# Optimization experiments

Measured on AMD Instinct MI355X. Metric: run time of the kernel, lower is better.

The kernel has to match this reference:

```python
import jax, jax.numpy as jnp
import numpy as np

N_NODES = 50000
N_EDGES = 800000
D_IN = 512
HIDDEN = 32
HEADS = 4
N_CLASSES = 40
NEG_SLOPE = 0.2


def gat_layer(x, W, a_src, a_dst, b, src, dst, num_nodes, concat):
    # x: [N, D], W: [D, H, C], a_src/a_dst: [H, C], b: [H*C] or [C]
    h = jnp.einsum('nd,dhc->nhc', x, W)  # [N, H, C]
    # attention logits per edge (edge j->i with j=src, i=dst)
    e = jnp.sum(h[src] * a_src, axis=-1) + jnp.sum(h[dst] * a_dst, axis=-1)  # [E, H]
    e = jnp.where(e > 0, e, NEG_SLOPE * e)  # leaky_relu
    # segment softmax over incoming edges of each dst node
    m = jax.ops.segment_max(e, dst, num_segments=num_nodes)  # [N, H]
    ex = jnp.exp(e - m[dst])
    denom = jax.ops.segment_sum(ex, dst, num_segments=num_nodes)
    alpha = ex / (denom[dst] + 1e-9)  # [E, H]
    # weighted scatter-aggregate of neighbor features
    out = jax.ops.segment_sum(alpha[:, :, None] * h[src], dst, num_segments=num_nodes)  # [N, H, C]
    if concat:
        out = out.reshape(num_nodes, -1)  # [N, H*C]
    else:
        out = out.mean(axis=1)  # [N, C]
    return out + b, alpha


def setup_inputs() -> dict:
    key = jax.random.key(0)
    ks = jax.random.split(key, 12)
    x = jax.random.normal(ks[0], (N_NODES, D_IN), dtype=jnp.float32)
    src = jax.random.randint(ks[1], (N_EDGES,), 0, N_NODES, dtype=jnp.int32)
    dst = jax.random.randint(ks[2], (N_EDGES,), 0, N_NODES, dtype=jnp.int32)
    s1 = 1.0 / np.sqrt(D_IN)
    W1 = jax.random.normal(ks[3], (D_IN, HEADS, HIDDEN), dtype=jnp.float32) * s1
    a_src1 = jax.random.normal(ks[4], (HEADS, HIDDEN), dtype=jnp.float32) * 0.1
    a_dst1 = jax.random.normal(ks[5], (HEADS, HIDDEN), dtype=jnp.float32) * 0.1
    b1 = jnp.zeros((HEADS * HIDDEN,), dtype=jnp.float32)
    d2 = HEADS * HIDDEN
    s2 = 1.0 / np.sqrt(d2)
    W2 = jax.random.normal(ks[6], (d2, 1, N_CLASSES), dtype=jnp.float32) * s2
    a_src2 = jax.random.normal(ks[7], (1, N_CLASSES), dtype=jnp.float32) * 0.1
    a_dst2 = jax.random.normal(ks[8], (1, N_CLASSES), dtype=jnp.float32) * 0.1
    b2 = jnp.zeros((N_CLASSES,), dtype=jnp.float32)
    return {"x": x, "src": src, "dst": dst,
            "W1": W1, "a_src1": a_src1, "a_dst1": a_dst1, "b1": b1,
            "W2": W2, "a_src2": a_src2, "a_dst2": a_dst2, "b2": b2}


def reference(x, src, dst, W1, a_src1, a_dst1, b1, W2, a_src2, a_dst2, b2):
    n = x.shape[0]
    # add self loops (standard in GATConv)
    loops = jnp.arange(n, dtype=src.dtype)
    s = jnp.concatenate([src, loops])
    d = jnp.concatenate([dst, loops])
    h1, _attn = gat_layer(x, W1, a_src1, a_dst1, b1, s, d, n, concat=True)
    h1 = jax.nn.elu(h1)
    h2, _ = gat_layer(h1, W2, a_src2, a_dst2, b2, s, d, n, concat=False)
    return jax.nn.softmax(h2, axis=-1)
```

## Files before the change

kernel.cpp:

```cpp
#include <hip/hip_runtime.h>
#include <hip/hip_bf16.h>
#include <math.h>

#define NN 50000
#define NE 800000
#define ET 850000
#define DIN 512
#define F1 128
#define NC 40
#define NEG 0.2f
#define CAP 128
#define SCAN_NB ((NN + 255) / 256)

typedef __attribute__((ext_vector_type(8))) short s16x8;
typedef __attribute__((ext_vector_type(4))) float f32x4;

__device__ inline unsigned short bfh(float f) {
    __hip_bfloat16 h = __float2bfloat16(f);
    return __builtin_bit_cast(unsigned short, h);
}
__device__ inline float bff(unsigned short u) {
    unsigned int x = (unsigned int)u << 16;
    return __builtin_bit_cast(float, x);
}

__device__ inline void split8(f32x4 v0, f32x4 v1, s16x8* hi, s16x8* lo) {
    float f[8] = {v0.x, v0.y, v0.z, v0.w, v1.x, v1.y, v1.z, v1.w};
    #pragma unroll
    for (int j = 0; j < 8; ++j) {
        unsigned short h = bfh(f[j]);
        (*hi)[j] = (short)h;
        (*lo)[j] = (short)bfh(f[j] - bff(h));
    }
}

__device__ inline void gl16(const void* g, void* l) {
    __builtin_amdgcn_global_load_lds((const __attribute__((address_space(1))) unsigned int*)g,
                                     (__attribute__((address_space(3))) unsigned int*)l, 16, 0, 0);
}

__global__ void prep_kernel(const float* __restrict__ W1,
        const float* __restrict__ W2, int* __restrict__ deg,
        unsigned short* __restrict__ Wh1T, unsigned short* __restrict__ Wl1T,
        unsigned short* __restrict__ Wh2T, unsigned short* __restrict__ Wl2T) {
    int i = blockIdx.x * blockDim.x + threadIdx.x;
    if (i < NN) deg[i] = 0;
    if (i < DIN * F1) {
        int k = i >> 7, c = i & 127;
        float w = W1[i];
        unsigned short h = bfh(w);
        unsigned short l = bfh(w - bff(h));
        Wh1T[c * DIN + k] = h;
        Wl1T[c * DIN + k] = l;
    }
    if (i < 48 * 128) {
        int c = i >> 7, k = i & 127;
        float w = (c < NC) ? W2[k * NC + c] : 0.f;
        unsigned short h = bfh(w);
        unsigned short l = bfh(w - bff(h));
        Wh2T[c * 128 + k] = h;
        Wl2T[c * 128 + k] = l;
    }
}

__global__ void hist_kernel(const int* __restrict__ dst, int* __restrict__ deg) {
    int e = blockIdx.x * blockDim.x + threadIdx.x;
    if (e >= ET) return;
    int d = (e < NE) ? dst[e] : (e - NE);
    atomicAdd(&deg[d], 1);
}

__global__ __launch_bounds__(256) void partial_kernel(const int* __restrict__ deg,
        int* __restrict__ bsum) {
    __shared__ int red[4];
    int i = blockIdx.x * 256 + threadIdx.x;
    int v = (i < NN) ? deg[i] : 0;
    #pragma unroll
    for (int o = 1; o < 64; o <<= 1) v += __shfl_xor(v, o);
    if ((threadIdx.x & 63) == 0) red[threadIdx.x >> 6] = v;
    __syncthreads();
    if (threadIdx.x == 0) bsum[blockIdx.x] = red[0] + red[1] + red[2] + red[3];
}

__global__ __launch_bounds__(256) void scanp_kernel(const int* __restrict__ bsum,
        int* __restrict__ bbase) {
    __shared__ int s[256];
    int t = threadIdx.x;
    s[t] = (t < SCAN_NB) ? bsum[t] : 0;
    __syncthreads();
    #pragma unroll
    for (int o = 1; o < 256; o <<= 1) {
        int v = (t >= o) ? s[t - o] : 0;
        __syncthreads();
        s[t] += v;
        __syncthreads();
    }
    if (t < SCAN_NB) bbase[t] = (t == 0) ? 0 : s[t - 1];
}

__global__ __launch_bounds__(256) void emit_kernel(const int* __restrict__ deg,
        const int* __restrict__ bbase, int* __restrict__ off, int* __restrict__ cur) {
    __shared__ int s[256];
    int t = threadIdx.x;
    int i = blockIdx.x * 256 + t;
    int d = (i < NN) ? deg[i] : 0;
    s[t] = d;
    __syncthreads();
    #pragma unroll
    for (int o = 1; o < 256; o <<= 1) {
        int v = (t >= o) ? s[t - o] : 0;
        __syncthreads();
        s[t] += v;
        __syncthreads();
    }
    int o0 = bbase[blockIdx.x] + s[t] - d;
    if (i < NN) { off[i] = o0; cur[i] = o0; }
    if (i == NN - 1) off[NN] = o0 + d;
}

__global__ void scatter_kernel(const int* __restrict__ src, const int* __restrict__ dst,
        int* __restrict__ cur, int* __restrict__ ssorted) {
    int e = blockIdx.x * blockDim.x + threadIdx.x;
    if (e >= ET) return;
    int s = (e < NE) ? src[e] : (e - NE);
    int d = (e < NE) ? dst[e] : (e - NE);
    int pos = atomicAdd(&cur[d], 1);
    ssorted[pos] = s;
}

__global__ __launch_bounds__(256) void gemm1_mfma(const float* __restrict__ X,
        const unsigned short* __restrict__ BhT, const unsigned short* __restrict__ BlT,
        const float* __restrict__ a_src, const float* __restrict__ a_dst,
        float* __restrict__ H, float* __restrict__ s1s, float* __restrict__ s1d) {
    __shared__ char lds[49152];
    char* ldsAh = lds;
    char* ldsAl = lds + 8192;
    char* ldsBh = lds + 16384;
    char* ldsBl = lds + 32768;
    const int tid = threadIdx.x;
    const int wid = tid >> 6, lane = tid & 63;
    const int wm = wid >> 1, wn = wid & 1;
    const int l15 = lane & 15, lg = lane >> 4;
    const int row0 = blockIdx.x * 64;

    const int arow = tid >> 2;
    const int akc  = (tid & 3) * 16;
    const int asw  = (arow & 7) << 4;
    int agr = row0 + arow; if (agr > NN - 1) agr = NN - 1;
    const float* aptr = X + (long)agr * DIN + akc;

    f32x4 acc[2][4];
    #pragma unroll
    for (int mi = 0; mi < 2; ++mi)
        #pragma unroll
        for (int ni = 0; ni < 4; ++ni) acc[mi][ni] = (f32x4)(0.f);

    for (int k0 = 0; k0 < DIN; k0 += 64) {
        #pragma unroll
        for (int p = 0; p < 4; ++p) {
            int q = p * 256 + tid;
            int dstoff = (p * 256 + wid * 64) << 4;
            int rr = q >> 3;
            int w = (q & 7) << 4;
            int sw = (rr & 7) << 4;
            long sb = (long)rr * (DIN * 2) + k0 * 2 + (w ^ sw);
            gl16((const char*)BhT + sb, ldsBh + dstoff);
            gl16((const char*)BlT + sb, ldsBl + dstoff);
        }
        {
            f32x4 v0 = *(const f32x4*)(aptr + k0);
            f32x4 v1 = *(const f32x4*)(aptr + k0 + 4);
            f32x4 v2 = *(const f32x4*)(aptr + k0 + 8);
            f32x4 v3 = *(const f32x4*)(aptr + k0 + 12);
            s16x8 h0, l0, h1, l1;
            split8(v0, v1, &h0, &l0);
            split8(v2, v3, &h1, &l1);
            int b0 = arow * 128 + ((akc * 2) ^ asw);
            int b1 = arow * 128 + ((akc * 2 + 16) ^ asw);
            *(s16x8*)(ldsAh + b0) = h0;
            *(s16x8*)(ldsAh + b1) = h1;
            *(s16x8*)(ldsAl + b0) = l0;
            *(s16x8*)(ldsAl + b1) = l1;
        }
        __syncthreads();
        #pragma unroll
        for (int ks = 0; ks < 2; ++ks) {
            s16x8 ah[2], al[2], bh[4], bl[4];
            #pragma unroll
            for (int mi = 0; mi < 2; ++mi) {
                int row = wm * 32 + mi * 16 + l15;
                int sw = (row & 7) << 4;
                int kb = (ks * 32 + lg * 8) * 2;
                ah[mi] = *(const s16x8*)(ldsAh + row * 128 + (kb ^ sw));
                al[mi] = *(const s16x8*)(ldsAl + row * 128 + (kb ^ sw));
            }
            #pragma unroll
            for (int ni = 0; ni < 4; ++ni) {
                int col = wn * 64 + ni * 16 + l15;
                int sw = (col & 7) << 4;
                int kb = (ks * 32 + lg * 8) * 2;
                bh[ni] = *(const s16x8*)(ldsBh + col * 128 + (kb ^ sw));
                bl[ni] = *(const s16x8*)(ldsBl + col * 128 + (kb ^ sw));
            }
            #pragma unroll
            for (int mi = 0; mi < 2; ++mi)
                #pragma unroll
                for (int ni = 0; ni < 4; ++ni) {
                    acc[mi][ni] = __builtin_amdgcn_mfma_f32_16x16x32_bf16(ah[mi], bh[ni], acc[mi][ni], 0, 0, 0);
                    acc[mi][ni] = __builtin_amdgcn_mfma_f32_16x16x32_bf16(ah[mi], bl[ni], acc[mi][ni], 0, 0, 0);
                    acc[mi][ni] = __builtin_amdgcn_mfma_f32_16x16x32_bf16(al[mi], bh[ni], acc[mi][ni], 0, 0, 0);
                }
        }
        __syncthreads();
    }

    #pragma unroll
    for (int mi = 0; mi < 2; ++mi)
        #pragma unroll
        for (int ni = 0; ni < 4; ++ni) {
            int col = wn * 64 + ni * 16 + l15;
            #pragma unroll
            for (int r = 0; r < 4; ++r) {
                int grow = row0 + wm * 32 + mi * 16 + lg * 4 + r;
                if (grow < NN) H[(long)grow * F1 + col] = acc[mi][ni][r];
            }
        }
    float av[4], bv[4];
    #pragma unroll
    for (int ni = 0; ni < 4; ++ni) {
        int col = wn * 64 + ni * 16 + l15;
        av[ni] = a_src[col];
        bv[ni] = a_dst[col];
    }
    #pragma unroll
    for (int mi = 0; mi < 2; ++mi)
        #pragma unroll
        for (int hl = 0; hl < 2; ++hl) {
            #pragma unroll
            for (int r = 0; r < 4; ++r) {
                float t1 = acc[mi][2 * hl][r] * av[2 * hl] + acc[mi][2 * hl + 1][r] * av[2 * hl + 1];
                float t2 = acc[mi][2 * hl][r] * bv[2 * hl] + acc[mi][2 * hl + 1][r] * bv[2 * hl + 1];
                #pragma unroll
                for (int o = 1; o < 16; o <<= 1) {
                    t1 += __shfl_xor(t1, o);
                    t2 += __shfl_xor(t2, o);
                }
                int grow = row0 + wm * 32 + mi * 16 + lg * 4 + r;
                if (l15 == 0 && grow < NN) {
                    int head = 2 * wn + hl;
                    s1s[grow * 4 + head] = t1;
                    s1d[grow * 4 + head] = t2;
                }
            }
        }
}

__global__ __launch_bounds__(256) void gemm2_mfma(const float* __restrict__ H1,
        const unsigned short* __restrict__ B2h, const unsigned short* __restrict__ B2l,
        const float* __restrict__ a_src, const float* __restrict__ a_dst,
        float* __restrict__ Z, float* __restrict__ s2s, float* __restrict__ s2d) {
    __shared__ char lds[57344];
    char* ldsA  = lds;
    char* ldsBh = lds + 32768;
    char* ldsBl = lds + 45056;
    const int tid = threadIdx.x;
    const int wid = tid >> 6, lane = tid & 63;
    const int l15 = lane & 15, lg = lane >> 4;
    const int row0 = blockIdx.x * 64;

    #pragma unroll
    for (int p = 0; p < 8; ++p) {
        int q = p * 256 + tid;
        int row = q >> 5;
        int w = (q & 31) << 4;
        int sw = (row & 7) << 4;
        int gr = row0 + row; if (gr > NN - 1) gr = NN - 1;
        gl16((const char*)(H1 + (long)gr * F1) + (w ^ sw), ldsA + ((p * 256 + wid * 64) << 4));
    }
    #pragma unroll
    for (int p = 0; p < 3; ++p) {
        int q = p * 256 + tid;
        int rr = q >> 4;
        int w = (q & 15) << 4;
        int sw = (rr & 7) << 4;
        int dstoff = (p * 256 + wid * 64) << 4;
        gl16((const char*)B2h + rr * 256 + (w ^ sw), ldsBh + dstoff);
        gl16((const char*)B2l + rr * 256 + (w ^ sw), ldsBl + dstoff);
    }
    __syncthreads();

    f32x4 acc[3];
    #pragma unroll
    for (int ni = 0; ni < 3; ++ni) acc[ni] = (f32x4)(0.f);

    #pragma unroll
    for (int ks = 0; ks < 4; ++ks) {
        int row = wid * 16 + l15;
        int sw = (row & 7) << 4;
        int kb = (ks * 32 + lg * 8) * 4;
        f32x4 v0 = *(const f32x4*)(ldsA + row * 512 + ((kb)      ^ sw));
        f32x4 v1 = *(const f32x4*)(ldsA + row * 512 + ((kb + 16) ^ sw));
        s16x8 ah, al;
        split8(v0, v1, &ah, &al);
        #pragma unroll
        for (int ni = 0; ni < 3; ++ni) {
            int cc = ni * 16 + l15;
            int swb = (cc & 7) << 4;
            int kb2 = (ks * 32 + lg * 8) * 2;
            s16x8 bh = *(const s16x8*)(ldsBh + cc * 256 + (kb2 ^ swb));
            s16x8 bl = *(const s16x8*)(ldsBl + cc * 256 + (kb2 ^ swb));
            acc[ni] = __builtin_amdgcn_mfma_f32_16x16x32_bf16(ah, bh, acc[ni], 0, 0, 0);
            acc[ni] = __builtin_amdgcn_mfma_f32_16x16x32_bf16(ah, bl, acc[ni], 0, 0, 0);
            acc[ni] = __builtin_amdgcn_mfma_f32_16x16x32_bf16(al, bh, acc[ni], 0, 0, 0);
        }
    }

    float av[3], bv[3];
    #pragma unroll
    for (int ni = 0; ni < 3; ++ni) {
        int cc = ni * 16 + l15;
        av[ni] = (cc < NC) ? a_src[cc] : 0.f;
        bv[ni] = (cc < NC) ? a_dst[cc] : 0.f;
    }
    #pragma unroll
    for (int r = 0; r < 4; ++r) {
        int grow = row0 + wid * 16 + lg * 4 + r;
        bool ok = grow < NN;
        float t1 = acc[0][r] * av[0] + acc[1][r] * av[1] + acc[2][r] * av[2];
        float t2 = acc[0][r] * bv[0] + acc[1][r] * bv[1] + acc[2][r] * bv[2];
        #pragma unroll
        for (int o = 1; o < 16; o <<= 1) {
            t1 += __shfl_xor(t1, o);
            t2 += __shfl_xor(t2, o);
        }
        #pragma unroll
        for (int ni = 0; ni < 3; ++ni) {
            int cc = ni * 16 + l15;
            if (ok && cc < NC) Z[(long)grow * NC + cc] = acc[ni][r];
        }
        if (ok && l15 == 0) { s2s[grow] = t1; s2d[grow] = t2; }
    }
}

__global__ __launch_bounds__(256) void fusedagg1_kernel(
        const int* __restrict__ off, const int* __restrict__ ssorted,
        const float* __restrict__ ssrc, const float* __restrict__ sdst,
        const float* __restrict__ H, const float* __restrict__ b,
        float* __restrict__ O) {
    __shared__ int idx_lds[4][CAP];
    __shared__ __align__(16) float e_lds[4][CAP][4];
    const int nd = threadIdx.x >> 6;
    int n = blockIdx.x * 4 + nd;
    if (n >= NN) return;
    const int lane = threadIdx.x & 63;
    const int base = off[n];
    const int deg  = off[n + 1] - base;
    const float4 vd = *(const float4*)(sdst + (long)n * 4);

    float m0 = -1e30f, m1 = -1e30f, m2 = -1e30f, m3 = -1e30f;
    for (int k = lane; k < deg; k += 64) {
        int s = ssorted[base + k];
        float4 vs = *(const float4*)(ssrc + (long)s * 4);
        float x0 = vs.x + vd.x; x0 = (x0 > 0.f) ? x0 : NEG * x0;
        float x1 = vs.y + vd.y; x1 = (x1 > 0.f) ? x1 : NEG * x1;
        float x2 = vs.z + vd.z; x2 = (x2 > 0.f) ? x2 : NEG * x2;
        float x3 = vs.w + vd.w; x3 = (x3 > 0.f) ? x3 : NEG * x3;
        if (k < CAP) {
            idx_lds[nd][k] = s;
            *(f32x4*)&e_lds[nd][k][0] = (f32x4){x0, x1, x2, x3};
        }
        m0 = fmaxf(m0, x0); m1 = fmaxf(m1, x1);
        m2 = fmaxf(m2, x2); m3 = fmaxf(m3, x3);
    }
    #pragma unroll
    for (int o = 1; o < 64; o <<= 1) {
        m0 = fmaxf(m0, __shfl_xor(m0, o));
        m1 = fmaxf(m1, __shfl_xor(m1, o));
        m2 = fmaxf(m2, __shfl_xor(m2, o));
        m3 = fmaxf(m3, __shfl_xor(m3, o));
    }
    float t0 = 0.f, t1 = 0.f, t2 = 0.f, t3 = 0.f;
    for (int k = lane; k < deg; k += 64) {
        float x0, x1, x2, x3;
        if (k < CAP) {
            f32x4 v = *(const f32x4*)&e_lds[nd][k][0];
            x0 = v.x; x1 = v.y; x2 = v.z; x3 = v.w;
        } else {
            int s = ssorted[base + k];
            float4 vs = *(const float4*)(ssrc + (long)s * 4);
            x0 = vs.x + vd.x; x0 = (x0 > 0.f) ? x0 : NEG * x0;
            x1 = vs.y + vd.y; x1 = (x1 > 0.f) ? x1 : NEG * x1;
            x2 = vs.z + vd.z; x2 = (x2 > 0.f) ? x2 : NEG * x2;
            x3 = vs.w + vd.w; x3 = (x3 > 0.f) ? x3 : NEG * x3;
        }
        float e0 = __expf(x0 - m0), e1 = __expf(x1 - m1);
        float e2 = __expf(x2 - m2), e3 = __expf(x3 - m3);
        if (k < CAP) *(f32x4*)&e_lds[nd][k][0] = (f32x4){e0, e1, e2, e3};
        t0 += e0; t1 += e1; t2 += e2; t3 += e3;
    }
    #pragma unroll
    for (int o = 1; o < 64; o <<= 1) {
        t0 += __shfl_xor(t0, o); t1 += __shfl_xor(t1, o);
        t2 += __shfl_xor(t2, o); t3 += __shfl_xor(t3, o);
    }
    const int g = lane >> 4;
    const int l = lane & 15;
    const int hd = l >> 2;
    const float mh  = (hd == 0) ? m0 : (hd == 1) ? m1 : (hd == 2) ? m2 : m3;
    const float th  = (hd == 0) ? t0 : (hd == 1) ? t1 : (hd == 2) ? t2 : t3;
    const float ih  = 1.f / (th + 1e-9f);
    const float vdh = (hd == 0) ? vd.x : (hd == 1) ? vd.y : (hd == 2) ? vd.z : vd.w;
    const int c0 = l * 8;
    f32x4 accA = (f32x4)(0.f), accB = (f32x4)(0.f);
    const int kend = (deg < CAP) ? deg : CAP;
    for (int k = g; k < kend; k += 4) {
        int s = idx_lds[nd][k];
        float e = e_lds[nd][k][hd];
        const float* hp = H + (long)s * F1 + c0;
        f32x4 h0 = *(const f32x4*)(hp);
        f32x4 h1 = *(const f32x4*)(hp + 4);
        accA += (f32x4)(e) * h0;
        accB += (f32x4)(e) * h1;
    }
    for (int k = CAP + g; k < deg; k += 4) {
        int s = ssorted[base + k];
        float4 vs = *(const float4*)(ssrc + (long)s * 4);
        float x = ((hd == 0) ? vs.x : (hd == 1) ? vs.y : (hd == 2) ? vs.z : vs.w) + vdh;
        x = (x > 0.f) ? x : NEG * x;
        float e = __expf(x - mh);
        const float* hp = H + (long)s * F1 + c0;
        f32x4 h0 = *(const f32x4*)(hp);
        f32x4 h1 = *(const f32x4*)(hp + 4);
        accA += (f32x4)(e) * h0;
        accB += (f32x4)(e) * h1;
    }
    #pragma unroll
    for (int o = 16; o < 64; o <<= 1) {
        accA.x += __shfl_xor(accA.x, o); accA.y += __shfl_xor(accA.y, o);
        accA.z += __shfl_xor(accA.z, o); accA.w += __shfl_xor(accA.w, o);
        accB.x += __shfl_xor(accB.x, o); accB.y += __shfl_xor(accB.y, o);
        accB.z += __shfl_xor(accB.z, o); accB.w += __shfl_xor(accB.w, o);
    }
    if (g == 0) {
        f32x4 bbA = *(const f32x4*)(b + c0);
        f32x4 bbB = *(const f32x4*)(b + c0 + 4);
        f32x4 vA = accA * (f32x4)(ih) + bbA;
        f32x4 vB = accB * (f32x4)(ih) + bbB;
        vA.x = (vA.x > 0.f) ? vA.x : expm1f(vA.x);
        vA.y = (vA.y > 0.f) ? vA.y : expm1f(vA.y);
        vA.z = (vA.z > 0.f) ? vA.z : expm1f(vA.z);
        vA.w = (vA.w > 0.f) ? vA.w : expm1f(vA.w);
        vB.x = (vB.x > 0.f) ? vB.x : expm1f(vB.x);
        vB.y = (vB.y > 0.f) ? vB.y : expm1f(vB.y);
        vB.z = (vB.z > 0.f) ? vB.z : expm1f(vB.z);
        vB.w = (vB.w > 0.f) ? vB.w : expm1f(vB.w);
        *(f32x4*)(O + (long)n * F1 + c0)     = vA;
        *(f32x4*)(O + (long)n * F1 + c0 + 4) = vB;
    }
}

__global__ __launch_bounds__(256) void fusedagg2_kernel(
        const int* __restrict__ off, const int* __restrict__ ssorted,
        const float* __restrict__ ssrc, const float* __restrict__ sdst,
        const float* __restrict__ Z, const float* __restrict__ b,
        float* __restrict__ out) {
    __shared__ int   idx_lds[4][CAP];
    __shared__ float e_lds[4][CAP];
    const int nd = threadIdx.x >> 6;
    int n = blockIdx.x * 4 + nd;
    if (n >= NN) return;
    const int lane = threadIdx.x & 63;
    const int base = off[n];
    const int deg  = off[n + 1] - base;
    const float sdn = sdst[n];

    float m = -1e30f;
    for (int k = lane; k < deg; k += 64) {
        int s = ssorted[base + k];
        float x = ssrc[s] + sdn;
        x = (x > 0.f) ? x : NEG * x;
        if (k < CAP) { idx_lds[nd][k] = s; e_lds[nd][k] = x; }
        m = fmaxf(m, x);
    }
    #pragma unroll
    for (int o = 1; o < 64; o <<= 1) m = fmaxf(m, __shfl_xor(m, o));
    float t = 0.f;
    for (int k = lane; k < deg; k += 64) {
        float x;
        if (k < CAP) x = e_lds[nd][k];
        else {
            int s = ssorted[base + k];
            x = ssrc[s] + sdn;
            x = (x > 0.f) ? x : NEG * x;
        }
        float e = __expf(x - m);
        if (k < CAP) e_lds[nd][k] = e;
        t += e;
    }
    #pragma unroll
    for (int o = 1; o < 64; o <<= 1) t += __shfl_xor(t, o);
    const float inv = 1.f / (t + 1e-9f);

    const int g = lane >> 3;
    const int l = lane & 7;
    const int c0 = l * 5;
    float a0 = 0.f, a1 = 0.f, a2 = 0.f, a3 = 0.f, a4 = 0.f;
    const int kend = (deg < CAP) ? deg : CAP;
    for (int k = g; k < kend; k += 8) {
        int s = idx_lds[nd][k];
        float e = e_lds[nd][k];
        const float* zp = Z + (long)s * NC + c0;
        a0 += e * zp[0]; a1 += e * zp[1]; a2 += e * zp[2];
        a3 += e * zp[3]; a4 += e * zp[4];
    }
    for (int k = CAP + g; k < deg; k += 8) {
        int s = ssorted[base + k];
        float x = ssrc[s] + sdn;
        x = (x > 0.f) ? x : NEG * x;
        float e = __expf(x - m);
        const float* zp = Z + (long)s * NC + c0;
        a0 += e * zp[0]; a1 += e * zp[1]; a2 += e * zp[2];
        a3 += e * zp[3]; a4 += e * zp[4];
    }
    #pragma unroll
    for (int o = 8; o < 64; o <<= 1) {
        a0 += __shfl_xor(a0, o); a1 += __shfl_xor(a1, o);
        a2 += __shfl_xor(a2, o); a3 += __shfl_xor(a3, o);
        a4 += __shfl_xor(a4, o);
    }
    if (g == 0) {
        float v0 = a0 * inv + b[c0 + 0];
        float v1 = a1 * inv + b[c0 + 1];
        float v2 = a2 * inv + b[c0 + 2];
        float v3 = a3 * inv + b[c0 + 3];
        float v4 = a4 * inv + b[c0 + 4];
        float mx = fmaxf(fmaxf(fmaxf(v0, v1), fmaxf(v2, v3)), v4);
        #pragma unroll
        for (int o = 1; o < 8; o <<= 1) mx = fmaxf(mx, __shfl_xor(mx, o));
        float e0 = __expf(v0 - mx), e1 = __expf(v1 - mx), e2 = __expf(v2 - mx);
        float e3 = __expf(v3 - mx), e4 = __expf(v4 - mx);
        float s = e0 + e1 + e2 + e3 + e4;
        #pragma unroll
        for (int o = 1; o < 8; o <<= 1) s += __shfl_xor(s, o);
        float is = 1.f / s;
        float* op = out + (long)n * NC + c0;
        op[0] = e0 * is; op[1] = e1 * is; op[2] = e2 * is;
        op[3] = e3 * is; op[4] = e4 * is;
    }
}

extern "C" void kernel_launch(void* const* d_in, const int* in_sizes, int n_in,
                              void* d_out, int out_size, void* d_ws, size_t ws_size,
                              hipStream_t stream) {
    const float* x      = (const float*)d_in[0];
    const int*   src    = (const int*)  d_in[1];
    const int*   dst    = (const int*)  d_in[2];
    const float* W1     = (const float*)d_in[3];
    const float* a_src1 = (const float*)d_in[4];
    const float* a_dst1 = (const float*)d_in[5];
    const float* b1     = (const float*)d_in[6];
    const float* W2     = (const float*)d_in[7];
    const float* a_src2 = (const float*)d_in[8];
    const float* a_dst2 = (const float*)d_in[9];
    const float* b2     = (const float*)d_in[10];
    float* out = (float*)d_out;

    float* ws   = (float*)d_ws;
    float* hpre = ws;
    float* s1s  = hpre + 6400000;
    float* s1d  = s1s + 200000;
    float* h1   = s1d + 200000;
    float* z2   = h1 + 6400000;
    float* s2s  = z2 + 2000000;
    float* s2d  = s2s + 50000;
    int*   deg     = (int*)(s2d + 50000);
    int*   off     = deg + 50000;
    int*   cur     = off + 50008;
    int*   ssorted = cur + 50000;
    int*   bsum    = ssorted + 850000;
    int*   bbase   = bsum + 256;
    unsigned short* Wh1T = (unsigned short*)(bbase + 256);
    unsigned short* Wl1T = Wh1T + 65536;
    unsigned short* Wh2T = Wl1T + 65536;
    unsigned short* Wl2T = Wh2T + 6144;

    prep_kernel<<<(DIN * F1 + 255) / 256, 256, 0, stream>>>(W1, W2, deg, Wh1T, Wl1T, Wh2T, Wl2T);

    hist_kernel<<<(ET + 255) / 256, 256, 0, stream>>>(dst, deg);
    partial_kernel<<<SCAN_NB, 256, 0, stream>>>(deg, bsum);
    scanp_kernel<<<1, 256, 0, stream>>>(bsum, bbase);
    emit_kernel<<<SCAN_NB, 256, 0, stream>>>(deg, bbase, off, cur);
    scatter_kernel<<<(ET + 255) / 256, 256, 0, stream>>>(src, dst, cur, ssorted);

    gemm1_mfma<<<(NN + 63) / 64, 256, 0, stream>>>(x, Wh1T, Wl1T, a_src1, a_dst1, hpre, s1s, s1d);
    fusedagg1_kernel<<<(NN + 3) / 4, 256, 0, stream>>>(off, ssorted, s1s, s1d, hpre, b1, h1);

    gemm2_mfma<<<(NN + 63) / 64, 256, 0, stream>>>(h1, Wh2T, Wl2T, a_src2, a_dst2, z2, s2s, s2d);
    fusedagg2_kernel<<<(NN + 3) / 4, 256, 0, stream>>>(off, ssorted, s2s, s2d, z2, b2, out);
}
```

Baseline: 401.2 us.

## Store node features as fp16 and pre-split aggregated hidden into bf16 hi/lo

The projected features H and Z are now stored in fp16 instead of fp32, which halves the bytes read by the random gathers in both aggregation kernels. The first aggregation kernel now writes its output as bf16 hi/lo pairs, so gemm2 loads ready-made operands and no longer splits fp32 values in LDS. This lowers gather bandwidth and gemm2 load work, at the cost of fp16 rounding in the intermediate features and a small precision risk in the final output.

```diff
diff --git a/kernel.cpp b/kernel.cpp
--- a/kernel.cpp
+++ b/kernel.cpp
@@ -14,6 +14,7 @@
 
 typedef __attribute__((ext_vector_type(8))) short s16x8;
 typedef __attribute__((ext_vector_type(4))) float f32x4;
+typedef __attribute__((ext_vector_type(8))) _Float16 f16x8;
 
 __device__ inline unsigned short bfh(float f) {
     __hip_bfloat16 h = __float2bfloat16(f);
@@ -131,7 +132,7 @@
 __global__ __launch_bounds__(256) void gemm1_mfma(const float* __restrict__ X,
         const unsigned short* __restrict__ BhT, const unsigned short* __restrict__ BlT,
         const float* __restrict__ a_src, const float* __restrict__ a_dst,
-        float* __restrict__ H, float* __restrict__ s1s, float* __restrict__ s1d) {
+        _Float16* __restrict__ H, float* __restrict__ s1s, float* __restrict__ s1d) {
     __shared__ char lds[49152];
     char* ldsAh = lds;
     char* ldsAl = lds + 8192;
@@ -222,7 +223,7 @@
             #pragma unroll
             for (int r = 0; r < 4; ++r) {
                 int grow = row0 + wm * 32 + mi * 16 + lg * 4 + r;
-                if (grow < NN) H[(long)grow * F1 + col] = acc[mi][ni][r];
+                if (grow < NN) H[(long)grow * F1 + col] = (_Float16)acc[mi][ni][r];
             }
         }
     float av[4], bv[4];
@@ -255,12 +256,14 @@
         }
 }
 
-__global__ __launch_bounds__(256) void gemm2_mfma(const float* __restrict__ H1,
+__global__ __launch_bounds__(256) void gemm2_mfma(
+        const unsigned short* __restrict__ H1h, const unsigned short* __restrict__ H1l,
         const unsigned short* __restrict__ B2h, const unsigned short* __restrict__ B2l,
         const float* __restrict__ a_src, const float* __restrict__ a_dst,
-        float* __restrict__ Z, float* __restrict__ s2s, float* __restrict__ s2d) {
+        _Float16* __restrict__ Z, float* __restrict__ s2s, float* __restrict__ s2d) {
     __shared__ char lds[57344];
-    char* ldsA  = lds;
+    char* ldsAh = lds;
+    char* ldsAl = lds + 16384;
     char* ldsBh = lds + 32768;
     char* ldsBl = lds + 45056;
     const int tid = threadIdx.x;
@@ -269,13 +272,15 @@
     const int row0 = blockIdx.x * 64;
 
     #pragma unroll
-    for (int p = 0; p < 8; ++p) {
+    for (int p = 0; p < 4; ++p) {
         int q = p * 256 + tid;
-        int row = q >> 5;
-        int w = (q & 31) << 4;
-        int sw = (row & 7) << 4;
-        int gr = row0 + row; if (gr > NN - 1) gr = NN - 1;
-        gl16((const char*)(H1 + (long)gr * F1) + (w ^ sw), ldsA + ((p * 256 + wid * 64) << 4));
+        int rr = q >> 4;
+        int w = (q & 15) << 4;
+        int sw = (rr & 7) << 4;
+        int gr = row0 + rr; if (gr > NN - 1) gr = NN - 1;
+        int dstoff = (p * 256 + wid * 64) << 4;
+        gl16((const char*)(H1h + (long)gr * F1) + (w ^ sw), ldsAh + dstoff);
+        gl16((const char*)(H1l + (long)gr * F1) + (w ^ sw), ldsAl + dstoff);
     }
     #pragma unroll
     for (int p = 0; p < 3; ++p) {
@@ -297,18 +302,15 @@
     for (int ks = 0; ks < 4; ++ks) {
         int row = wid * 16 + l15;
         int sw = (row & 7) << 4;
-        int kb = (ks * 32 + lg * 8) * 4;
-        f32x4 v0 = *(const f32x4*)(ldsA + row * 512 + ((kb)      ^ sw));
-        f32x4 v1 = *(const f32x4*)(ldsA + row * 512 + ((kb + 16) ^ sw));
-        s16x8 ah, al;
-        split8(v0, v1, &ah, &al);
+        int kb = (ks * 32 + lg * 8) * 2;
+        s16x8 ah = *(const s16x8*)(ldsAh + row * 256 + (kb ^ sw));
+        s16x8 al = *(const s16x8*)(ldsAl + row * 256 + (kb ^ sw));
         #pragma unroll
         for (int ni = 0; ni < 3; ++ni) {
             int cc = ni * 16 + l15;
             int swb = (cc & 7) << 4;
-            int kb2 = (ks * 32 + lg * 8) * 2;
-            s16x8 bh = *(const s16x8*)(ldsBh + cc * 256 + (kb2 ^ swb));
-            s16x8 bl = *(const s16x8*)(ldsBl + cc * 256 + (kb2 ^ swb));
+            s16x8 bh = *(const s16x8*)(ldsBh + cc * 256 + (kb ^ swb));
+            s16x8 bl = *(const s16x8*)(ldsBl + cc * 256 + (kb ^ swb));
             acc[ni] = __builtin_amdgcn_mfma_f32_16x16x32_bf16(ah, bh, acc[ni], 0, 0, 0);
             acc[ni] = __builtin_amdgcn_mfma_f32_16x16x32_bf16(ah, bl, acc[ni], 0, 0, 0);
             acc[ni] = __builtin_amdgcn_mfma_f32_16x16x32_bf16(al, bh, acc[ni], 0, 0, 0);
@@ -336,7 +338,7 @@
         #pragma unroll
         for (int ni = 0; ni < 3; ++ni) {
             int cc = ni * 16 + l15;
-            if (ok && cc < NC) Z[(long)grow * NC + cc] = acc[ni][r];
+            if (ok && cc < NC) Z[(long)grow * NC + cc] = (_Float16)acc[ni][r];
         }
         if (ok && l15 == 0) { s2s[grow] = t1; s2d[grow] = t2; }
     }
@@ -345,8 +347,8 @@
 __global__ __launch_bounds__(256) void fusedagg1_kernel(
         const int* __restrict__ off, const int* __restrict__ ssorted,
         const float* __restrict__ ssrc, const float* __restrict__ sdst,
-        const float* __restrict__ H, const float* __restrict__ b,
-        float* __restrict__ O) {
+        const _Float16* __restrict__ H, const float* __restrict__ b,
+        unsigned short* __restrict__ Oh, unsigned short* __restrict__ Ol) {
     __shared__ int idx_lds[4][CAP];
     __shared__ __align__(16) float e_lds[4][CAP][4];
     const int nd = threadIdx.x >> 6;
@@ -416,11 +418,11 @@
     for (int k = g; k < kend; k += 4) {
         int s = idx_lds[nd][k];
         float e = e_lds[nd][k][hd];
-        const float* hp = H + (long)s * F1 + c0;
-        f32x4 h0 = *(const f32x4*)(hp);
-        f32x4 h1 = *(const f32x4*)(hp + 4);
-        accA += (f32x4)(e) * h0;
-        accB += (f32x4)(e) * h1;
+        f16x8 hv = *(const f16x8*)(H + (long)s * F1 + c0);
+        accA.x += e * (float)hv[0]; accA.y += e * (float)hv[1];
+        accA.z += e * (float)hv[2]; accA.w += e * (float)hv[3];
+        accB.x += e * (float)hv[4]; accB.y += e * (float)hv[5];
+        accB.z += e * (float)hv[6]; accB.w += e * (float)hv[7];
     }
     for (int k = CAP + g; k < deg; k += 4) {
         int s = ssorted[base + k];
@@ -428,11 +430,11 @@
         float x = ((hd == 0) ? vs.x : (hd == 1) ? vs.y : (hd == 2) ? vs.z : vs.w) + vdh;
         x = (x > 0.f) ? x : NEG * x;
         float e = __expf(x - mh);
-        const float* hp = H + (long)s * F1 + c0;
-        f32x4 h0 = *(const f32x4*)(hp);
-        f32x4 h1 = *(const f32x4*)(hp + 4);
-        accA += (f32x4)(e) * h0;
-        accB += (f32x4)(e) * h1;
+        f16x8 hv = *(const f16x8*)(H + (long)s * F1 + c0);
+        accA.x += e * (float)hv[0]; accA.y += e * (float)hv[1];
+        accA.z += e * (float)hv[2]; accA.w += e * (float)hv[3];
+        accB.x += e * (float)hv[4]; accB.y += e * (float)hv[5];
+        accB.z += e * (float)hv[6]; accB.w += e * (float)hv[7];
     }
     #pragma unroll
     for (int o = 16; o < 64; o <<= 1) {
@@ -454,15 +456,17 @@
         vB.y = (vB.y > 0.f) ? vB.y : expm1f(vB.y);
         vB.z = (vB.z > 0.f) ? vB.z : expm1f(vB.z);
         vB.w = (vB.w > 0.f) ? vB.w : expm1f(vB.w);
-        *(f32x4*)(O + (long)n * F1 + c0)     = vA;
-        *(f32x4*)(O + (long)n * F1 + c0 + 4) = vB;
+        s16x8 hi, lo;
+        split8(vA, vB, &hi, &lo);
+        *(s16x8*)(Oh + (long)n * F1 + c0) = hi;
+        *(s16x8*)(Ol + (long)n * F1 + c0) = lo;
     }
 }
 
 __global__ __launch_bounds__(256) void fusedagg2_kernel(
         const int* __restrict__ off, const int* __restrict__ ssorted,
         const float* __restrict__ ssrc, const float* __restrict__ sdst,
-        const float* __restrict__ Z, const float* __restrict__ b,
+        const _Float16* __restrict__ Z, const float* __restrict__ b,
         float* __restrict__ out) {
     __shared__ int   idx_lds[4][CAP];
     __shared__ float e_lds[4][CAP];
@@ -509,18 +513,18 @@
     for (int k = g; k < kend; k += 8) {
         int s = idx_lds[nd][k];
         float e = e_lds[nd][k];
-        const float* zp = Z + (long)s * NC + c0;
-        a0 += e * zp[0]; a1 += e * zp[1]; a2 += e * zp[2];
-        a3 += e * zp[3]; a4 += e * zp[4];
+        const _Float16* zp = Z + (long)s * NC + c0;
+        a0 += e * (float)zp[0]; a1 += e * (float)zp[1]; a2 += e * (float)zp[2];
+        a3 += e * (float)zp[3]; a4 += e * (float)zp[4];
     }
     for (int k = CAP + g; k < deg; k += 8) {
         int s = ssorted[base + k];
         float x = ssrc[s] + sdn;
         x = (x > 0.f) ? x : NEG * x;
         float e = __expf(x - m);
-        const float* zp = Z + (long)s * NC + c0;
-        a0 += e * zp[0]; a1 += e * zp[1]; a2 += e * zp[2];
-        a3 += e * zp[3]; a4 += e * zp[4];
+        const _Float16* zp = Z + (long)s * NC + c0;
+        a0 += e * (float)zp[0]; a1 += e * (float)zp[1]; a2 += e * (float)zp[2];
+        a3 += e * (float)zp[3]; a4 += e * (float)zp[4];
     }
     #pragma unroll
     for (int o = 8; o < 64; o <<= 1) {
@@ -566,14 +570,15 @@
     float* out = (float*)d_out;
 
     float* ws   = (float*)d_ws;
-    float* hpre = ws;
-    float* s1s  = hpre + 6400000;
+    float* s1s  = ws;
     float* s1d  = s1s + 200000;
-    float* h1   = s1d + 200000;
-    float* z2   = h1 + 6400000;
-    float* s2s  = z2 + 2000000;
+    float* s2s  = s1d + 200000;
     float* s2d  = s2s + 50000;
-    int*   deg     = (int*)(s2d + 50000);
+    _Float16* H16 = (_Float16*)(s2d + 50000);
+    unsigned short* h1h = (unsigned short*)(H16 + 6400000);
+    unsigned short* h1l = h1h + 6400000;
+    _Float16* z16 = (_Float16*)(h1l + 6400000);
+    int*   deg     = (int*)(z16 + 2000000);
     int*   off     = deg + 50000;
     int*   cur     = off + 50008;
     int*   ssorted = cur + 50000;
@@ -592,9 +597,9 @@
     emit_kernel<<<SCAN_NB, 256, 0, stream>>>(deg, bbase, off, cur);
     scatter_kernel<<<(ET + 255) / 256, 256, 0, stream>>>(src, dst, cur, ssorted);
 
-    gemm1_mfma<<<(NN + 63) / 64, 256, 0, stream>>>(x, Wh1T, Wl1T, a_src1, a_dst1, hpre, s1s, s1d);
-    fusedagg1_kernel<<<(NN + 3) / 4, 256, 0, stream>>>(off, ssorted, s1s, s1d, hpre, b1, h1);
-
-    gemm2_mfma<<<(NN + 63) / 64, 256, 0, stream>>>(h1, Wh2T, Wl2T, a_src2, a_dst2, z2, s2s, s2d);
-    fusedagg2_kernel<<<(NN + 3) / 4, 256, 0, stream>>>(off, ssorted, s2s, s2d, z2, b2, out);
-}
+    gemm1_mfma<<<(NN + 63) / 64, 256, 0, stream>>>(x, Wh1T, Wl1T, a_src1, a_dst1, H16, s1s, s1d);
+    fusedagg1_kernel<<<(NN + 3) / 4, 256, 0, stream>>>(off, ssorted, s1s, s1d, H16, b1, h1h, h1l);
+
+    gemm2_mfma<<<(NN + 63) / 64, 256, 0, stream>>>(h1h, h1l, Wh2T, Wl2T, a_src2, a_dst2, z16, s2s, s2d);
+    fusedagg2_kernel<<<(NN + 3) / 4, 256, 0, stream>>>(off, ssorted, s2s, s2d, z16, b2, out);
+}
```

Measured after the change: 371.6 us. 7.4% less time.
